# Kernel optimization log

Measured on AMD Instinct MI355X. Metric: run time of the kernel, lower is better.

Reference implementation:

```python
import jax, jax.numpy as jnp
import numpy as np

RADIUS = 0.4
K = 32
EPS = 1e-5


def ball_query(xyz, new_xyz, radius, k):
    """xyz: (B,N,3), new_xyz: (B,M,3) -> idx (B,M,k) int32.
    Replicates CUDA ball_query: first k points within radius (in index order),
    padded with the first found index."""
    N = xyz.shape[1]
    # squared distances (B,M,N)
    d2 = jnp.sum((new_xyz[:, :, None, :] - xyz[:, None, :, :]) ** 2, axis=-1)
    within = d2 < radius * radius
    order = jnp.arange(N, dtype=jnp.int32)
    key = jnp.where(within, order[None, None, :], N)
    idx_sorted = jnp.argsort(key, axis=-1)[..., :k].astype(jnp.int32)  # (B,M,k)
    cnt = within.sum(axis=-1)  # (B,M)
    first = idx_sorted[..., :1]
    slot = jnp.arange(k)[None, None, :]
    return jnp.where(slot < cnt[..., None], idx_sorted, first)


def gather_bmk(x_bnc, idx):
    """x_bnc: (B,N,C), idx: (B,M,K) -> (B,M,K,C)"""
    return jnp.take_along_axis(x_bnc[:, None, :, :], idx[..., None], axis=2)


def conv_bn_relu(x, w, b, gamma, beta):
    """x: (B,Cin,M,K); w: (Cout,Cin). 1x1 Conv2d + BatchNorm2d (train stats) + ReLU."""
    x = jnp.einsum('bcmk,oc->bomk', x, w) + b[None, :, None, None]
    mu = x.mean(axis=(0, 2, 3), keepdims=True)
    var = x.var(axis=(0, 2, 3), keepdims=True)
    x = gamma[None, :, None, None] * (x - mu) * jax.lax.rsqrt(var + EPS) + beta[None, :, None, None]
    return jax.nn.relu(x)


def setup_inputs() -> dict:
    key = jax.random.key(0)
    ks = jax.random.split(key, 16)
    B, N, C, M = 4, 16384, 128, 1024
    mlp = [131, 128, 128, 256]
    inp = {
        'points_xyz': jax.random.normal(ks[0], (B, N, 3), dtype=jnp.float32),
        'features': jax.random.normal(ks[1], (B, C, N), dtype=jnp.float32),
        'indices': jax.random.randint(ks[2], (B, M), 0, N, dtype=jnp.int32),
    }
    for i in range(3):
        cin, cout = mlp[i], mlp[i + 1]
        inp[f'w{i+1}'] = jax.random.normal(ks[3 + 4 * i], (cout, cin), dtype=jnp.float32) / np.sqrt(cin)
        inp[f'b{i+1}'] = jnp.zeros((cout,), dtype=jnp.float32)
        inp[f'g{i+1}'] = jnp.ones((cout,), dtype=jnp.float32)
        inp[f'beta{i+1}'] = jnp.zeros((cout,), dtype=jnp.float32)
    return inp


def reference(points_xyz, features, indices,
              w1, b1, g1, beta1, w2, b2, g2, beta2, w3, b3, g3, beta3):
    # sample centers: new_xyz (B,M,3)
    new_xyz = jnp.take_along_axis(points_xyz, indices[..., None], axis=1)
    # ball query + group
    idx = ball_query(points_xyz, new_xyz, RADIUS, K)            # (B,M,K)
    grouped_xyz = gather_bmk(points_xyz, idx) - new_xyz[:, :, None, :]  # (B,M,K,3)
    grouped_feat = gather_bmk(features.transpose(0, 2, 1), idx)         # (B,M,K,C)
    x = jnp.concatenate([grouped_xyz, grouped_feat], axis=-1)           # (B,M,K,3+C)
    x = x.transpose(0, 3, 1, 2)                                         # (B,3+C,M,K)
    # shared MLP (1x1 Conv2d + BN + ReLU)
    x = conv_bn_relu(x, w1, b1, g1, beta1)
    x = conv_bn_relu(x, w2, b2, g2, beta2)
    x = conv_bn_relu(x, w3, b3, g3, beta3)
    # max pool over K -> (B, Cout, M)
    new_features = x.max(axis=-1)
    return new_xyz, new_features
```

## Files before the change

kernel.cpp:

```cpp
#include <hip/hip_runtime.h>

#define B_ 4
#define N_ 16384
#define C_ 128
#define M_ 1024
#define K_ 32
#define NTOT (B_*M_*K_)
#define RAD2 0.16f
#define EPS_ 1e-5f

typedef unsigned short ushort_t;
typedef __bf16 bf16x8 __attribute__((ext_vector_type(8)));
typedef float f32x4 __attribute__((ext_vector_type(4)));

__device__ __forceinline__ float b2f(ushort_t u){
  unsigned int x = ((unsigned int)u) << 16;
  return __builtin_bit_cast(float, x);
}
__device__ __forceinline__ ushort_t f2b(float f){
  unsigned int u = __builtin_bit_cast(unsigned int, f);
  unsigned int r = (u + 0x7FFFu + ((u >> 16) & 1u)) >> 16;
  return (ushort_t)r;
}

__global__ __launch_bounds__(256) void ball_query_k(
    const float* __restrict__ xyz, const int* __restrict__ indices,
    float* __restrict__ new_xyz, int* __restrict__ idx)
{
  __shared__ float pts[2][512*3];
  int t = threadIdx.x;
  int wv = t >> 6, lane = t & 63;
  int g = blockIdx.x*4 + wv;
  int b = g >> 10;
  const float* pb = xyz + (size_t)b*N_*3;
  int qi = indices[g];
  float qx = pb[qi*3+0], qy = pb[qi*3+1], qz = pb[qi*3+2];
  if (lane < 3) new_xyz[g*3 + lane] = pb[qi*3 + lane];

  float2 st0, st1, st2;
  {
    const float2* src = (const float2*)pb + t*3;
    st0 = src[0]; st1 = src[1]; st2 = src[2];
    float2* dst = (float2*)(&pts[0][0]) + t*3;
    dst[0] = st0; dst[1] = st1; dst[2] = st2;
  }
  __syncthreads();

  int cnt = 0, firstIdx = 0;
  int* op = idx + g*K_;
  for (int chunk = 0; chunk < 32; chunk++){
    int cur = chunk & 1;
    bool have_next = (chunk + 1 < 32);
    if (have_next){
      const float2* src = (const float2*)(pb + (chunk+1)*512*3) + t*3;
      st0 = src[0]; st1 = src[1]; st2 = src[2];
    }
    if (cnt < K_){
      int base = chunk*512;
      float px[8], py[8], pz[8];
      #pragma unroll
      for (int r = 0; r < 8; r++){
        const float* p = &pts[cur][(r*64 + lane)*3];
        px[r] = p[0]; py[r] = p[1]; pz[r] = p[2];
      }
      #pragma unroll
      for (int r = 0; r < 8; r++){
        float dx = px[r]-qx, dy = py[r]-qy, dz = pz[r]-qz;
        bool within = (dx*dx + dy*dy + dz*dz) < RAD2;
        unsigned long long mask = __ballot(within);
        if (cnt == 0 && mask) firstIdx = base + r*64 + __builtin_ctzll(mask);
        if (within){
          int slot = cnt + __popcll(mask & ((1ull << lane) - 1ull));
          if (slot < K_) op[slot] = base + r*64 + lane;
        }
        cnt += __popcll(mask);
      }
    }
    if (have_next){
      float2* dst = (float2*)(&pts[1-cur][0]) + t*3;
      dst[0] = st0; dst[1] = st1; dst[2] = st2;
    }
    if (__syncthreads_and(cnt >= K_)) break;
  }
  if (cnt < K_){
    for (int s = cnt + lane; s < K_; s += 64) op[s] = firstIdx;
  }
}

__global__ __launch_bounds__(256) void transpose_feat_k(
    const float* __restrict__ feat, ushort_t* __restrict__ ftr_t)
{
  __shared__ float T[32][133];
  int bi = blockIdx.x;
  int b = bi >> 9, ntile = bi & 511;
  int n0 = ntile * 32;
  int t = threadIdx.x;
  int nl = t & 31;
  #pragma unroll
  for (int ci = 0; ci < 16; ci++){
    int c = ci*8 + (t >> 5);
    T[nl][c] = feat[((size_t)b*C_ + c)*N_ + n0 + nl];
  }
  __syncthreads();
  #pragma unroll
  for (int ii = 0; ii < 2; ii++){
    int v = ii*256 + t;
    int n2 = v >> 4, seg = v & 15;
    union { ushort_t u[8]; uint4 q; } pk;
    #pragma unroll
    for (int j = 0; j < 8; j++) pk.u[j] = f2b(T[n2][seg*8 + j]);
    *(uint4*)(ftr_t + ((size_t)b*N_ + n0 + n2)*C_ + seg*8) = pk.q;
  }
}

__global__ __launch_bounds__(256) void prep_w_k(
    const float* __restrict__ w1, const float* __restrict__ w2, const float* __restrict__ w3,
    ushort_t* __restrict__ W1b, ushort_t* __restrict__ W2b, ushort_t* __restrict__ W3b)
{
  const int T1 = 128*160, T2 = 128*128, T3 = 256*128;
  for (int e = blockIdx.x*256 + threadIdx.x; e < T1+T2+T3; e += gridDim.x*256){
    if (e < T1){
      int o = e / 160, c = e % 160;
      float v = 0.f;
      if (c < 128) v = w1[o*131 + 3 + c];
      else if (c < 131) v = w1[o*131 + (c - 128)];
      W1b[e] = f2b(v);
    } else if (e < T1+T2){
      int e2 = e - T1;
      W2b[e2] = f2b(w2[e2]);
    } else {
      int e3 = e - T1 - T2;
      W3b[e3] = f2b(w3[e3]);
    }
  }
}

__global__ __launch_bounds__(256, 2) void conv1_k(
    const float* __restrict__ xyz, const ushort_t* __restrict__ ftr_t,
    const int* __restrict__ idx, const float* __restrict__ new_xyz,
    const ushort_t* __restrict__ W1b, const float* __restrict__ b1,
    ushort_t* __restrict__ Y1, float* __restrict__ sumO, float* __restrict__ sqO)
{
  __shared__ alignas(16) ushort_t Xs[32*168];
  __shared__ alignas(16) float Ys[32*132];
  int t = threadIdx.x;
  int wv = t >> 6, lane = t & 63, quad = lane >> 4, l15 = lane & 15;
  int row = t >> 3, chunk = t & 7;

  if (t < 128){
    int rr = t >> 2, cc = t & 3;
    *(uint4*)(Xs + rr*168 + 128 + cc*8) = make_uint4(0,0,0,0);
  }
  bf16x8 wf[2][5];
  #pragma unroll
  for (int nt = 0; nt < 2; nt++)
    #pragma unroll
    for (int kt = 0; kt < 5; kt++)
      wf[nt][kt] = *(const bf16x8*)(W1b + (wv*32 + nt*16 + l15)*160 + kt*32 + quad*8);
  float bs_r[2] = { b1[wv*32 + l15], b1[wv*32 + 16 + l15] };
  float s[2] = {0.f,0.f}, s2[2] = {0.f,0.f};

  const int GPB = 8;
  int g0 = blockIdx.x * GPB;
  for (int i = 0; i < GPB; i++){
    int g = g0 + i;
    int b = g >> 10;
    int n = idx[g*K_ + row];
    const ushort_t* src = ftr_t + ((size_t)b*N_ + n)*C_ + chunk*16;
    uint4 q0 = *(const uint4*)src;
    uint4 q1 = *(const uint4*)(src + 8);
    *(uint4*)(Xs + row*168 + chunk*16) = q0;
    *(uint4*)(Xs + row*168 + chunk*16 + 8) = q1;
    if (t < 32){
      int n2 = idx[g*K_ + t];
      const float* pp = xyz + ((size_t)b*N_ + n2)*3;
      const float* qq = new_xyz + (size_t)g*3;
      unsigned int u0 = (unsigned int)f2b(pp[0]-qq[0]) | ((unsigned int)f2b(pp[1]-qq[1]) << 16);
      unsigned int u1 = (unsigned int)f2b(pp[2]-qq[2]);
      *(uint2*)(Xs + t*168 + 128) = make_uint2(u0, u1);
    }
    __syncthreads();
    bf16x8 af[2][5];
    #pragma unroll
    for (int mt = 0; mt < 2; mt++)
      #pragma unroll
      for (int kt = 0; kt < 5; kt++)
        af[mt][kt] = *(const bf16x8*)(Xs + (mt*16 + l15)*168 + kt*32 + quad*8);
    f32x4 acc[2][2];
    #pragma unroll
    for (int nt = 0; nt < 2; nt++){ acc[nt][0] = (f32x4){0,0,0,0}; acc[nt][1] = (f32x4){0,0,0,0}; }
    #pragma unroll
    for (int nt = 0; nt < 2; nt++)
      #pragma unroll
      for (int kt = 0; kt < 5; kt++){
        acc[nt][0] = __builtin_amdgcn_mfma_f32_16x16x32_bf16(af[0][kt], wf[nt][kt], acc[nt][0], 0,0,0);
        acc[nt][1] = __builtin_amdgcn_mfma_f32_16x16x32_bf16(af[1][kt], wf[nt][kt], acc[nt][1], 0,0,0);
      }
    #pragma unroll
    for (int nt = 0; nt < 2; nt++){
      int o = wv*32 + nt*16 + l15;
      #pragma unroll
      for (int mt = 0; mt < 2; mt++)
        #pragma unroll
        for (int r = 0; r < 4; r++){
          float v = acc[nt][mt][r] + bs_r[nt];
          s[nt] += v; s2[nt] += v*v;
          Ys[(mt*16 + quad*4 + r)*132 + o] = v;
        }
    }
    __syncthreads();
    {
      const float* yp = &Ys[row*132 + chunk*16];
      f32x4 y0 = *(const f32x4*)(yp);
      f32x4 y1 = *(const f32x4*)(yp + 4);
      f32x4 y2 = *(const f32x4*)(yp + 8);
      f32x4 y3 = *(const f32x4*)(yp + 12);
      union { ushort_t u[8]; uint4 q; } p0, p1;
      #pragma unroll
      for (int j = 0; j < 4; j++){
        p0.u[j] = f2b(y0[j]); p0.u[4+j] = f2b(y1[j]);
        p1.u[j] = f2b(y2[j]); p1.u[4+j] = f2b(y3[j]);
      }
      ushort_t* dst = Y1 + ((size_t)g*K_ + row)*128 + chunk*16;
      *(uint4*)dst = p0.q;
      *(uint4*)(dst + 8) = p1.q;
    }
  }
  #pragma unroll
  for (int nt = 0; nt < 2; nt++){
    s[nt]  += __shfl_xor(s[nt], 16);  s[nt]  += __shfl_xor(s[nt], 32);
    s2[nt] += __shfl_xor(s2[nt], 16); s2[nt] += __shfl_xor(s2[nt], 32);
    if (quad == 0){
      int o = wv*32 + nt*16 + l15;
      atomicAdd(&sumO[o], s[nt]);
      atomicAdd(&sqO[o], s2[nt]);
    }
  }
}

template<int COUT, bool MAXMIN>
__global__ __launch_bounds__(256, 2) void convB_k(
    const ushort_t* __restrict__ Yin, const ushort_t* __restrict__ Wb,
    const float* __restrict__ bias, const float* __restrict__ g_bn,
    const float* __restrict__ beta_bn, const float* __restrict__ sumI,
    const float* __restrict__ sqI, ushort_t* __restrict__ Yout,
    unsigned int* __restrict__ Ymm, float* __restrict__ sumO, float* __restrict__ sqO)
{
  constexpr int NT = COUT/64;
  __shared__ alignas(16) ushort_t Xs[32*136];
  __shared__ alignas(16) float Ys[MAXMIN ? 4 : 32*132];
  int t = threadIdx.x;
  int wv = t >> 6, lane = t & 63, quad = lane >> 4, l15 = lane & 15;
  int row = t >> 3, chunk = t & 7;

  float a_r[16], d_r[16];
  #pragma unroll
  for (int j = 0; j < 16; j++){
    int c = chunk*16 + j;
    float mu  = sumI[c] * (1.f/NTOT);
    float var = sqI[c]  * (1.f/NTOT) - mu*mu;
    float a = g_bn[c] * rsqrtf(var + EPS_);
    a_r[j] = a; d_r[j] = beta_bn[c] - a*mu;
  }
  bf16x8 wf[NT][4];
  #pragma unroll
  for (int nt = 0; nt < NT; nt++)
    #pragma unroll
    for (int kt = 0; kt < 4; kt++)
      wf[nt][kt] = *(const bf16x8*)(Wb + (wv*(NT*16) + nt*16 + l15)*128 + kt*32 + quad*8);
  float bs_r[NT];
  #pragma unroll
  for (int nt = 0; nt < NT; nt++) bs_r[nt] = bias[wv*(NT*16) + nt*16 + l15];
  float s[NT], s2[NT];
  #pragma unroll
  for (int nt = 0; nt < NT; nt++){ s[nt] = 0.f; s2[nt] = 0.f; }

  const int GPB = 8;
  int g0 = blockIdx.x * GPB;
  uint4 r0, r1;
  {
    const ushort_t* src = Yin + ((size_t)g0*K_ + row)*128 + chunk*16;
    r0 = *(const uint4*)src; r1 = *(const uint4*)(src + 8);
  }
  for (int i = 0; i < GPB; i++){
    int g = g0 + i;
    union { ushort_t u[8]; uint4 q; } i0, i1, o0, o1;
    i0.q = r0; i1.q = r1;
    #pragma unroll
    for (int j = 0; j < 8; j++){
      o0.u[j] = f2b(fmaxf(a_r[j]  *b2f(i0.u[j]) + d_r[j],   0.f));
      o1.u[j] = f2b(fmaxf(a_r[8+j]*b2f(i1.u[j]) + d_r[8+j], 0.f));
    }
    *(uint4*)(Xs + row*136 + chunk*16) = o0.q;
    *(uint4*)(Xs + row*136 + chunk*16 + 8) = o1.q;
    if (i + 1 < GPB){
      const ushort_t* src = Yin + ((size_t)(g+1)*K_ + row)*128 + chunk*16;
      r0 = *(const uint4*)src; r1 = *(const uint4*)(src + 8);
    }
    __syncthreads();
    bf16x8 af[2][4];
    #pragma unroll
    for (int mt = 0; mt < 2; mt++)
      #pragma unroll
      for (int kt = 0; kt < 4; kt++)
        af[mt][kt] = *(const bf16x8*)(Xs + (mt*16 + l15)*136 + kt*32 + quad*8);
    f32x4 acc[NT][2];
    #pragma unroll
    for (int nt = 0; nt < NT; nt++){ acc[nt][0] = (f32x4){0,0,0,0}; acc[nt][1] = (f32x4){0,0,0,0}; }
    #pragma unroll
    for (int nt = 0; nt < NT; nt++)
      #pragma unroll
      for (int kt = 0; kt < 4; kt++){
        acc[nt][0] = __builtin_amdgcn_mfma_f32_16x16x32_bf16(af[0][kt], wf[nt][kt], acc[nt][0], 0,0,0);
        acc[nt][1] = __builtin_amdgcn_mfma_f32_16x16x32_bf16(af[1][kt], wf[nt][kt], acc[nt][1], 0,0,0);
      }
    if constexpr (!MAXMIN){
      #pragma unroll
      for (int nt = 0; nt < NT; nt++){
        int o = wv*(NT*16) + nt*16 + l15;
        #pragma unroll
        for (int mt = 0; mt < 2; mt++)
          #pragma unroll
          for (int r = 0; r < 4; r++){
            float v = acc[nt][mt][r] + bs_r[nt];
            s[nt] += v; s2[nt] += v*v;
            Ys[(mt*16 + quad*4 + r)*132 + o] = v;
          }
      }
      __syncthreads();
      const float* yp = &Ys[row*132 + chunk*16];
      f32x4 y0 = *(const f32x4*)(yp);
      f32x4 y1 = *(const f32x4*)(yp + 4);
      f32x4 y2 = *(const f32x4*)(yp + 8);
      f32x4 y3 = *(const f32x4*)(yp + 12);
      union { ushort_t u[8]; uint4 q; } p0, p1;
      #pragma unroll
      for (int j = 0; j < 4; j++){
        p0.u[j] = f2b(y0[j]); p0.u[4+j] = f2b(y1[j]);
        p1.u[j] = f2b(y2[j]); p1.u[4+j] = f2b(y3[j]);
      }
      ushort_t* dst = Yout + ((size_t)g*K_ + row)*128 + chunk*16;
      *(uint4*)dst = p0.q;
      *(uint4*)(dst + 8) = p1.q;
    } else {
      #pragma unroll
      for (int nt = 0; nt < NT; nt++){
        float v0 = acc[nt][0][0] + bs_r[nt];
        float mx = v0, mn = v0;
        s[nt] += v0; s2[nt] += v0*v0;
        #pragma unroll
        for (int mt = 0; mt < 2; mt++)
          #pragma unroll
          for (int r = 0; r < 4; r++){
            if (mt == 0 && r == 0) continue;
            float v = acc[nt][mt][r] + bs_r[nt];
            s[nt] += v; s2[nt] += v*v;
            mx = fmaxf(mx, v); mn = fminf(mn, v);
          }
        mx = fmaxf(mx, __shfl_xor(mx, 16)); mx = fmaxf(mx, __shfl_xor(mx, 32));
        mn = fminf(mn, __shfl_xor(mn, 16)); mn = fminf(mn, __shfl_xor(mn, 32));
        if (quad == 0){
          int o = wv*64 + nt*16 + l15;
          Ymm[(size_t)g*256 + o] = (unsigned int)f2b(mx) | ((unsigned int)f2b(mn) << 16);
        }
      }
      __syncthreads();
    }
  }
  #pragma unroll
  for (int nt = 0; nt < NT; nt++){
    s[nt]  += __shfl_xor(s[nt], 16);  s[nt]  += __shfl_xor(s[nt], 32);
    s2[nt] += __shfl_xor(s2[nt], 16); s2[nt] += __shfl_xor(s2[nt], 32);
    if (quad == 0){
      int o = wv*(NT*16) + nt*16 + l15;
      atomicAdd(&sumO[o], s[nt]);
      atomicAdd(&sqO[o], s2[nt]);
    }
  }
}

__global__ __launch_bounds__(256) void finalize_k(
    const unsigned int* __restrict__ Ymm, const float* __restrict__ g3,
    const float* __restrict__ beta3, const float* __restrict__ sum3,
    const float* __restrict__ sq3, float* __restrict__ out)
{
  __shared__ float T[16][264];
  __shared__ float abn[256], dbn[256];
  int t = threadIdx.x;
  int b = blockIdx.x >> 6;
  int m0 = (blockIdx.x & 63) * 16;
  {
    float mu  = sum3[t] * (1.f/NTOT);
    float var = sq3[t]  * (1.f/NTOT) - mu*mu;
    float a = g3[t] * rsqrtf(var + EPS_);
    abn[t] = a; dbn[t] = beta3[t] - a*mu;
  }
  __syncthreads();
  #pragma unroll
  for (int i = 0; i < 4; i++){
    int v4 = i*256 + t;
    int m = v4 >> 6, oq = (v4 & 63) * 4;
    uint4 w = *(const uint4*)(Ymm + ((size_t)(b*M_ + m0 + m))*256 + oq);
    unsigned int wsv[4] = {w.x, w.y, w.z, w.w};
    float r[4];
    #pragma unroll
    for (int j = 0; j < 4; j++){
      int o = oq + j;
      float mx = b2f((ushort_t)(wsv[j] & 0xffffu));
      float mn = b2f((ushort_t)(wsv[j] >> 16));
      float a = abn[o];
      float val = (a >= 0.f) ? (a*mx + dbn[o]) : (a*mn + dbn[o]);
      r[j] = fmaxf(val, 0.f);
    }
    *(f32x4*)(&T[m][oq]) = *(f32x4*)r;
  }
  __syncthreads();
  #pragma unroll
  for (int p = 0; p < 4; p++){
    int o = p*64 + (t >> 2), c = t & 3;
    float4 v = make_float4(T[c*4+0][o], T[c*4+1][o], T[c*4+2][o], T[c*4+3][o]);
    *(float4*)(out + ((size_t)(b*256 + o))*M_ + m0 + c*4) = v;
  }
}

extern "C" void kernel_launch(void* const* d_in, const int* in_sizes, int n_in,
                              void* d_out, int out_size, void* d_ws, size_t ws_size,
                              hipStream_t stream)
{
  (void)in_sizes; (void)n_in; (void)out_size; (void)ws_size;
  const float* xyz  = (const float*)d_in[0];
  const float* feat = (const float*)d_in[1];
  const int*   inds = (const int*)d_in[2];
  const float* w1 = (const float*)d_in[3];
  const float* b1 = (const float*)d_in[4];
  const float* g1 = (const float*)d_in[5];
  const float* be1= (const float*)d_in[6];
  const float* w2 = (const float*)d_in[7];
  const float* b2 = (const float*)d_in[8];
  const float* g2 = (const float*)d_in[9];
  const float* be2= (const float*)d_in[10];
  const float* w3 = (const float*)d_in[11];
  const float* b3 = (const float*)d_in[12];
  const float* g3 = (const float*)d_in[13];
  const float* be3= (const float*)d_in[14];

  char* ws = (char*)d_ws;
  float* stats = (float*)ws;
  float* s1sum = stats + 0*256;  float* s1sq = stats + 1*256;
  float* s2sum = stats + 2*256;  float* s2sq = stats + 3*256;
  float* s3sum = stats + 4*256;  float* s3sq = stats + 5*256;
  size_t off = 6*256*sizeof(float);
  int* idx = (int*)(ws + off);                off += (size_t)B_*M_*K_*4;
  ushort_t* ftr_t = (ushort_t*)(ws + off);    off += (size_t)B_*N_*C_*2;
  ushort_t* W1b = (ushort_t*)(ws + off);      off += 128*160*2;
  ushort_t* W2b = (ushort_t*)(ws + off);      off += 128*128*2;
  ushort_t* W3b = (ushort_t*)(ws + off);      off += 256*128*2;
  ushort_t* Y1 = (ushort_t*)(ws + off);       off += (size_t)NTOT*128*2;
  ushort_t* Y2 = (ushort_t*)(ws + off);       off += (size_t)NTOT*128*2;
  unsigned int* Ymm = (unsigned int*)(ws + off); off += (size_t)B_*M_*256*4;

  float* new_xyz  = (float*)d_out;
  float* out_feat = (float*)d_out + (size_t)B_*M_*3;

  hipMemsetAsync(stats, 0, 6*256*sizeof(float), stream);
  prep_w_k<<<272, 256, 0, stream>>>(w1, w2, w3, W1b, W2b, W3b);
  transpose_feat_k<<<2048, 256, 0, stream>>>(feat, ftr_t);
  ball_query_k<<<1024, 256, 0, stream>>>(xyz, inds, new_xyz, idx);
  conv1_k<<<512, 256, 0, stream>>>(xyz, ftr_t, idx, new_xyz, W1b, b1, Y1, s1sum, s1sq);
  convB_k<128,false><<<512, 256, 0, stream>>>(Y1, W2b, b2, g1, be1, s1sum, s1sq, Y2, nullptr, s2sum, s2sq);
  convB_k<256,true ><<<512, 256, 0, stream>>>(Y2, W3b, b3, g2, be2, s2sum, s2sq, nullptr, Ymm, s3sum, s3sq);
  finalize_k<<<256, 256, 0, stream>>>(Ymm, g3, be3, s3sum, s3sq, out_feat);
}
```

Before: 250.2 us.

## Rewrite ball query as per-wave register-streamed scan without shared memory

The ball query kernel stops staging points through double-buffered shared memory with block-wide barriers. Each wave now streams contiguous 8-point runs per lane straight from global memory into registers as float4 loads, prefetching the next chunk. A shuffle-based prefix scan orders the hits, and each wave exits on its own as soon as it has K neighbours instead of waiting on a block-wide vote. Contiguous per-lane ranges keep index order through the exclusive scan, but the kernel gives up shared-memory reuse across the block's four waves and adds scan overhead per chunk.

Result: faster. 227.6 us (-9.0%).

```diff
diff --git a/kernel.cpp b/kernel.cpp
--- a/kernel.cpp
+++ b/kernel.cpp
@@ -27,60 +27,70 @@
     const float* __restrict__ xyz, const int* __restrict__ indices,
     float* __restrict__ new_xyz, int* __restrict__ idx)
 {
-  __shared__ float pts[2][512*3];
   int t = threadIdx.x;
   int wv = t >> 6, lane = t & 63;
   int g = blockIdx.x*4 + wv;
   int b = g >> 10;
   const float* pb = xyz + (size_t)b*N_*3;
+  const float4* pb4 = (const float4*)pb;
   int qi = indices[g];
   float qx = pb[qi*3+0], qy = pb[qi*3+1], qz = pb[qi*3+2];
   if (lane < 3) new_xyz[g*3 + lane] = pb[qi*3 + lane];
 
-  float2 st0, st1, st2;
-  {
-    const float2* src = (const float2*)pb + t*3;
-    st0 = src[0]; st1 = src[1]; st2 = src[2];
-    float2* dst = (float2*)(&pts[0][0]) + t*3;
-    dst[0] = st0; dst[1] = st1; dst[2] = st2;
-  }
-  __syncthreads();
-
   int cnt = 0, firstIdx = 0;
   int* op = idx + g*K_;
-  for (int chunk = 0; chunk < 32; chunk++){
-    int cur = chunk & 1;
-    bool have_next = (chunk + 1 < 32);
-    if (have_next){
-      const float2* src = (const float2*)(pb + (chunk+1)*512*3) + t*3;
-      st0 = src[0]; st1 = src[1]; st2 = src[2];
-    }
-    if (cnt < K_){
-      int base = chunk*512;
-      float px[8], py[8], pz[8];
-      #pragma unroll
-      for (int r = 0; r < 8; r++){
-        const float* p = &pts[cur][(r*64 + lane)*3];
-        px[r] = p[0]; py[r] = p[1]; pz[r] = p[2];
-      }
-      #pragma unroll
-      for (int r = 0; r < 8; r++){
-        float dx = px[r]-qx, dy = py[r]-qy, dz = pz[r]-qz;
-        bool within = (dx*dx + dy*dy + dz*dz) < RAD2;
-        unsigned long long mask = __ballot(within);
-        if (cnt == 0 && mask) firstIdx = base + r*64 + __builtin_ctzll(mask);
-        if (within){
-          int slot = cnt + __popcll(mask & ((1ull << lane) - 1ull));
-          if (slot < K_) op[slot] = base + r*64 + lane;
-        }
-        cnt += __popcll(mask);
-      }
-    }
-    if (have_next){
-      float2* dst = (float2*)(&pts[1-cur][0]) + t*3;
-      dst[0] = st0; dst[1] = st1; dst[2] = st2;
-    }
-    if (__syncthreads_and(cnt >= K_)) break;
+
+  float4 buf0[6], buf1[6];
+  #pragma unroll
+  for (int i = 0; i < 6; i++) buf0[i] = pb4[lane*6 + i];
+
+  auto process = [&](const float4* buf, int chunk){
+    const float* f = (const float*)buf;
+    unsigned int local_mask = 0;
+    #pragma unroll
+    for (int j = 0; j < 8; j++){
+      float dx = f[j*3+0]-qx, dy = f[j*3+1]-qy, dz = f[j*3+2]-qz;
+      if (dx*dx + dy*dy + dz*dz < RAD2) local_mask |= (1u << j);
+    }
+    if (__ballot(local_mask != 0) == 0ull) return;
+    int base = chunk*512;
+    int lcnt = __popc(local_mask);
+    int incl = lcnt;
+    #pragma unroll
+    for (int d = 1; d < 64; d <<= 1){
+      int tt = __shfl_up(incl, d);
+      if (lane >= d) incl += tt;
+    }
+    int excl = incl - lcnt;
+    int total = __shfl(incl, 63);
+    if (cnt == 0){
+      int lf = local_mask ? (lane*8 + __builtin_ctz(local_mask)) : 0x7fffffff;
+      #pragma unroll
+      for (int d = 1; d < 64; d <<= 1) lf = min(lf, __shfl_xor(lf, d));
+      firstIdx = base + lf;
+    }
+    int sl = cnt + excl;
+    unsigned int m = local_mask;
+    while (m && sl < K_){
+      int j = __builtin_ctz(m); m &= m - 1u;
+      op[sl++] = base + lane*8 + j;
+    }
+    cnt += total;
+  };
+
+  for (int chunk = 0; chunk < 32; chunk += 2){
+    if (chunk + 1 < 32){
+      #pragma unroll
+      for (int i = 0; i < 6; i++) buf1[i] = pb4[(chunk+1)*384 + lane*6 + i];
+    }
+    process(buf0, chunk);
+    if (cnt >= K_) break;
+    if (chunk + 2 < 32){
+      #pragma unroll
+      for (int i = 0; i < 6; i++) buf0[i] = pb4[(chunk+2)*384 + lane*6 + i];
+    }
+    process(buf1, chunk + 1);
+    if (cnt >= K_) break;
   }
   if (cnt < K_){
     for (int s = cnt + lane; s < K_; s += 64) op[s] = firstIdx;
```
